# Kernel optimization log

Measured on AMD Instinct MI355X. Metric: run time of the kernel, lower is better.

Reference implementation:

```python
import jax, jax.numpy as jnp
import numpy as np

BLOCK = 128
QMAX = 127.0


def act_quant(x2d):
    # Per (row, 128-wide block) symmetric int8 quantization.
    # x2d: [M, K] -> q int8-valued [M, K], scales [M, K//BLOCK]
    M, K = x2d.shape
    xb = x2d.reshape(M, K // BLOCK, BLOCK)
    s = jnp.max(jnp.abs(xb), axis=-1) / QMAX            # [M, K//BLOCK]
    s = jnp.maximum(s, 1e-12)
    q = jnp.clip(jnp.round(xb / s[..., None]), -128.0, 127.0)
    return q, s  # q kept in fp32 (exact small ints)


def weight_quant(w):
    # w: [N, K] -> q [N, K], scales [N//BLOCK, K//BLOCK]
    N, K = w.shape
    wb = w.reshape(N // BLOCK, BLOCK, K // BLOCK, BLOCK)
    s = jnp.max(jnp.abs(wb), axis=(1, 3)) / QMAX        # [N//BLOCK, K//BLOCK]
    s = jnp.maximum(s, 1e-12)
    q = jnp.clip(jnp.round(wb / s[:, None, :, None]), -128.0, 127.0)
    return q.reshape(N, K), s


def setup_inputs() -> dict:
    key = jax.random.key(0)
    k1, k2, k3 = jax.random.split(key, 3)
    x = jax.random.normal(k1, (4, 2048, 4096), dtype=jnp.float32)
    weight = jax.random.normal(k2, (4096, 4096), dtype=jnp.float32) * 0.02
    bias = jax.random.normal(k3, (4096,), dtype=jnp.float32) * 0.02
    return {"x": x, "weight": weight, "bias": bias}


def reference(x, weight, bias):
    # Int8Linear.forward: block-quantize activation, int8 GEMM with
    # grouped dequant scales (equivalent to dequantize-then-matmul), add bias.
    orig_shape = x.shape
    K = weight.shape[1]
    N = weight.shape[0]
    x2d = x.reshape(-1, K)                              # [M, K]
    M = x2d.shape[0]

    xq, xs = act_quant(x2d)                             # [M,Kb,128], [M,Kb]
    wq, ws = weight_quant(weight)                       # [N,K],     [Nb,Kb]

    # Dequantize (exact factorization of the scaled int8 GEMM):
    # out[m,n] = sum_kb xs[m,kb]*ws[nb,kb] * sum_c xq[m,kb,c]*wq[n,kb,c]
    x_dq = (xq * xs[..., None]).reshape(M, K)
    wqb = wq.reshape(N // BLOCK, BLOCK, K // BLOCK, BLOCK)
    w_dq = (wqb * ws[:, None, :, None]).reshape(N, K)

    out = x_dq @ w_dq.T + bias                          # [M, N]
    return out.reshape(orig_shape[:-1] + (N,))
```

## Files before the change

kernel.cpp:

```cpp
#include <hip/hip_runtime.h>
#include <stdint.h>

#define K_DIM 4096
#define N_DIM 4096
#define KB    32
#define QMAXF 127.0f

typedef int v4i __attribute__((ext_vector_type(4)));

__device__ __forceinline__ void async_copy16(void* lds, const void* gptr) {
    __builtin_amdgcn_global_load_lds(
        (__attribute__((address_space(1))) void*)gptr,
        (__attribute__((address_space(3))) void*)lds, 16, 0, 0);
}

__global__ __launch_bounds__(256) void act_quant_kernel(
    const float* __restrict__ x, int8_t* __restrict__ xq,
    float* __restrict__ xs_t, int M)
{
    const int m = blockIdx.x;
    const int t = threadIdx.x;
    const float* xrow = x + (size_t)m * K_DIM;
    int8_t* qrow = xq + (size_t)m * K_DIM;

#pragma unroll
    for (int p = 0; p < 4; ++p) {
        const int base = p * 1024 + t * 4;
        float4 v = *(const float4*)(xrow + base);
        float a = fmaxf(fmaxf(fabsf(v.x), fabsf(v.y)), fmaxf(fabsf(v.z), fabsf(v.w)));
#pragma unroll
        for (int off = 1; off < 32; off <<= 1)
            a = fmaxf(a, __shfl_xor(a, off, 64));
        const float s = fmaxf(a / QMAXF, 1e-12f);
        const float inv = 1.0f / s;
        float q0 = fminf(fmaxf(rintf(v.x * inv), -128.f), 127.f);
        float q1 = fminf(fmaxf(rintf(v.y * inv), -128.f), 127.f);
        float q2 = fminf(fmaxf(rintf(v.z * inv), -128.f), 127.f);
        float q3 = fminf(fmaxf(rintf(v.w * inv), -128.f), 127.f);
        char4 pk;
        pk.x = (char)(int)q0; pk.y = (char)(int)q1;
        pk.z = (char)(int)q2; pk.w = (char)(int)q3;
        *(char4*)(qrow + base) = pk;
        if ((t & 31) == 0) {
            const int g = base >> 7;
            xs_t[(size_t)g * M + m] = s;
        }
    }
}

__global__ __launch_bounds__(256) void weight_quant_kernel(
    const float* __restrict__ w, int8_t* __restrict__ wq, float* __restrict__ ws)
{
    const int nb = blockIdx.x >> 5;
    const int kb = blockIdx.x & 31;
    const int t  = threadIdx.x;
    const int n0 = nb * 128, k0 = kb * 128;

    float4 vals[16];
    float a = 0.f;
#pragma unroll
    for (int ii = 0; ii < 16; ++ii) {
        const int e = ii * 1024 + t * 4;
        const int row = e >> 7, col = e & 127;
        float4 v = *(const float4*)(w + (size_t)(n0 + row) * K_DIM + k0 + col);
        vals[ii] = v;
        a = fmaxf(a, fmaxf(fmaxf(fabsf(v.x), fabsf(v.y)), fmaxf(fabsf(v.z), fabsf(v.w))));
    }
#pragma unroll
    for (int off = 1; off < 64; off <<= 1)
        a = fmaxf(a, __shfl_xor(a, off, 64));
    __shared__ float wred[4];
    if ((t & 63) == 0) wred[t >> 6] = a;
    __syncthreads();
    a = fmaxf(fmaxf(wred[0], wred[1]), fmaxf(wred[2], wred[3]));
    const float s = fmaxf(a / QMAXF, 1e-12f);
    const float inv = 1.0f / s;
    if (t == 0) ws[nb * KB + kb] = s;

#pragma unroll
    for (int ii = 0; ii < 16; ++ii) {
        const int e = ii * 1024 + t * 4;
        const int row = e >> 7, col = e & 127;
        float4 v = vals[ii];
        char4 pk;
        pk.x = (char)(int)fminf(fmaxf(rintf(v.x * inv), -128.f), 127.f);
        pk.y = (char)(int)fminf(fmaxf(rintf(v.y * inv), -128.f), 127.f);
        pk.z = (char)(int)fminf(fmaxf(rintf(v.z * inv), -128.f), 127.f);
        pk.w = (char)(int)fminf(fmaxf(rintf(v.w * inv), -128.f), 127.f);
        *(char4*)(wq + (size_t)(n0 + row) * K_DIM + k0 + col) = pk;
    }
}

__global__ __launch_bounds__(256, 3) void gemm_kernel(
    const int8_t* __restrict__ xq, const int8_t* __restrict__ wq,
    const float* __restrict__ xs_t, const float* __restrict__ ws,
    const float* __restrict__ bias, float* __restrict__ out, int M)
{
    __shared__ __align__(16) int8_t As[128 * 128];
    __shared__ __align__(16) int8_t Bs[128 * 128];
    __shared__ __align__(16) float  xs_s[KB * 128];
    __shared__ float ws_s[KB];

    const int t    = threadIdx.x;
    const int lane = t & 63;
    const int wave = t >> 6;
    const int nb   = blockIdx.x;
    const int n0   = nb * 128;
    const int m0   = blockIdx.y * 128;

#pragma unroll
    for (int i = 0; i < 4; ++i) {
        const int idx = t * 4 + i * 1024;
        const int kbi = idx >> 7, r = idx & 127;
        *(float4*)&xs_s[idx] = *(const float4*)&xs_t[(size_t)kbi * M + m0 + r];
    }
    if (t < KB) ws_s[t] = ws[nb * KB + t];

    const int wm    = (wave >> 1) * 64;
    const int wn    = (wave & 1) * 64;
    const int frow  = lane & 15;
    const int q     = lane >> 4;
    const int quad4 = q * 4;
    const int sw0   = ((q ^ (frow & 7)) * 16);

    float4 facc[4][4] = {};

    float bj[4];
#pragma unroll
    for (int j = 0; j < 4; ++j) bj[j] = bias[n0 + wn + j * 16 + frow];

    for (int kb = 0; kb < KB; ++kb) {
        __syncthreads();
        const int8_t* Ag = xq + (size_t)m0 * K_DIM + kb * 128;
        const int8_t* Bg = wq + (size_t)n0 * K_DIM + kb * 128;
#pragma unroll
        for (int it = 0; it < 4; ++it) {
            const int ci  = it * 256 + t;
            const int row = ci >> 3;
            const int c   = (ci & 7) ^ (row & 7);
            void* la = (void*)&As[(it * 256 + wave * 64) * 16];
            void* lb = (void*)&Bs[(it * 256 + wave * 64) * 16];
            async_copy16(la, Ag + (size_t)row * K_DIM + c * 16);
            async_copy16(lb, Bg + (size_t)row * K_DIM + c * 16);
        }
        __syncthreads();

        v4i a0[4], a1[4], b0[4], b1[4];
#pragma unroll
        for (int i = 0; i < 4; ++i) {
            a0[i] = *(const v4i*)&As[(wm + i * 16 + frow) * 128 + sw0];
            a1[i] = *(const v4i*)&As[(wm + i * 16 + frow) * 128 + (sw0 ^ 64)];
            b0[i] = *(const v4i*)&Bs[(wn + i * 16 + frow) * 128 + sw0];
            b1[i] = *(const v4i*)&Bs[(wn + i * 16 + frow) * 128 + (sw0 ^ 64)];
        }
        const float wskb = ws_s[kb];
#pragma unroll
        for (int i = 0; i < 4; ++i) {
            float4 xs4 = *(const float4*)&xs_s[kb * 128 + wm + i * 16 + quad4];
            const float s0 = xs4.x * wskb, s1 = xs4.y * wskb;
            const float s2 = xs4.z * wskb, s3 = xs4.w * wskb;
#pragma unroll
            for (int j = 0; j < 4; ++j) {
                v4i d = __builtin_amdgcn_mfma_i32_16x16x64_i8(a0[i], b0[j], (v4i){0, 0, 0, 0}, 0, 0, 0);
                d = __builtin_amdgcn_mfma_i32_16x16x64_i8(a1[i], b1[j], d, 0, 0, 0);
                facc[i][j].x += (float)d[0] * s0;
                facc[i][j].y += (float)d[1] * s1;
                facc[i][j].z += (float)d[2] * s2;
                facc[i][j].w += (float)d[3] * s3;
            }
        }
    }

#pragma unroll
    for (int i = 0; i < 4; ++i) {
#pragma unroll
        for (int r = 0; r < 4; ++r) {
            const int row = m0 + wm + i * 16 + quad4 + r;
            float* orow = out + (size_t)row * N_DIM + n0 + wn + frow;
#pragma unroll
            for (int j = 0; j < 4; ++j)
                orow[j * 16] = ((const float*)&facc[i][j])[r] + bj[j];
        }
    }
}

extern "C" void kernel_launch(void* const* d_in, const int* in_sizes, int n_in,
                              void* d_out, int out_size, void* d_ws, size_t ws_size,
                              hipStream_t stream)
{
    const float* x    = (const float*)d_in[0];
    const float* w    = (const float*)d_in[1];
    const float* bias = (const float*)d_in[2];
    float* out = (float*)d_out;
    const int M = in_sizes[0] / K_DIM;

    int8_t* xq  = (int8_t*)d_ws;
    int8_t* wqp = xq + (size_t)M * K_DIM;
    float*  xst = (float*)(wqp + (size_t)N_DIM * K_DIM);
    float*  wsp = xst + (size_t)KB * M;

    act_quant_kernel<<<M, 256, 0, stream>>>(x, xq, xst, M);
    weight_quant_kernel<<<(N_DIM / 128) * KB, 256, 0, stream>>>(w, wqp, wsp);
    gemm_kernel<<<dim3(N_DIM / 128, M / 128), 256, 0, stream>>>(
        xq, wqp, xst, wsp, bias, out, M);
}
```

Baseline: 446.1 us.

## Enlarge GEMM tile to 256x128 and batch activation-quant loads

The GEMM block tile grows from 128x128 to 256x128 rows. Each wave now computes 128x64 with 8x4 accumulators, so each loaded B tile is reused across twice as many rows and per-FLOP global/LDS traffic drops. Bias is folded into the accumulator init, and the scale accumulation uses explicit FMA. The activation quant kernel processes two rows per block and issues all eight loads before reducing, to raise memory-level parallelism. The cost is more registers and LDS per block, lowering occupancy (launch bounds go from 3 to 2) and leaving half as many GEMM blocks in the grid.

Measured after the change: 549.2 us. 1.23x slower.

```diff
diff --git a/kernel.cpp b/kernel.cpp
--- a/kernel.cpp
+++ b/kernel.cpp
@@ -18,31 +18,35 @@
     const float* __restrict__ x, int8_t* __restrict__ xq,
     float* __restrict__ xs_t, int M)
 {
-    const int m = blockIdx.x;
-    const int t = threadIdx.x;
+    const int t   = threadIdx.x;
+    const int r   = t >> 7;
+    const int tid = t & 127;
+    const int m   = blockIdx.x * 2 + r;
     const float* xrow = x + (size_t)m * K_DIM;
     int8_t* qrow = xq + (size_t)m * K_DIM;
 
-#pragma unroll
-    for (int p = 0; p < 4; ++p) {
-        const int base = p * 1024 + t * 4;
-        float4 v = *(const float4*)(xrow + base);
-        float a = fmaxf(fmaxf(fabsf(v.x), fabsf(v.y)), fmaxf(fabsf(v.z), fabsf(v.w)));
+    float4 v[8];
+#pragma unroll
+    for (int p = 0; p < 8; ++p)
+        v[p] = *(const float4*)(xrow + p * 512 + tid * 4);
+
+#pragma unroll
+    for (int p = 0; p < 8; ++p) {
+        float a = fmaxf(fmaxf(fabsf(v[p].x), fabsf(v[p].y)),
+                        fmaxf(fabsf(v[p].z), fabsf(v[p].w)));
 #pragma unroll
         for (int off = 1; off < 32; off <<= 1)
             a = fmaxf(a, __shfl_xor(a, off, 64));
         const float s = fmaxf(a / QMAXF, 1e-12f);
         const float inv = 1.0f / s;
-        float q0 = fminf(fmaxf(rintf(v.x * inv), -128.f), 127.f);
-        float q1 = fminf(fmaxf(rintf(v.y * inv), -128.f), 127.f);
-        float q2 = fminf(fmaxf(rintf(v.z * inv), -128.f), 127.f);
-        float q3 = fminf(fmaxf(rintf(v.w * inv), -128.f), 127.f);
         char4 pk;
-        pk.x = (char)(int)q0; pk.y = (char)(int)q1;
-        pk.z = (char)(int)q2; pk.w = (char)(int)q3;
-        *(char4*)(qrow + base) = pk;
-        if ((t & 31) == 0) {
-            const int g = base >> 7;
+        pk.x = (char)(int)fminf(fmaxf(rintf(v[p].x * inv), -128.f), 127.f);
+        pk.y = (char)(int)fminf(fmaxf(rintf(v[p].y * inv), -128.f), 127.f);
+        pk.z = (char)(int)fminf(fmaxf(rintf(v[p].z * inv), -128.f), 127.f);
+        pk.w = (char)(int)fminf(fmaxf(rintf(v[p].w * inv), -128.f), 127.f);
+        *(char4*)(qrow + p * 512 + tid * 4) = pk;
+        if ((tid & 31) == 0) {
+            const int g = p * 4 + (tid >> 5);
             xs_t[(size_t)g * M + m] = s;
         }
     }
@@ -91,14 +95,14 @@
     }
 }
 
-__global__ __launch_bounds__(256, 3) void gemm_kernel(
+__global__ __launch_bounds__(256, 2) void gemm_kernel(
     const int8_t* __restrict__ xq, const int8_t* __restrict__ wq,
     const float* __restrict__ xs_t, const float* __restrict__ ws,
     const float* __restrict__ bias, float* __restrict__ out, int M)
 {
-    __shared__ __align__(16) int8_t As[128 * 128];
+    __shared__ __align__(16) int8_t As[256 * 128];
     __shared__ __align__(16) int8_t Bs[128 * 128];
-    __shared__ __align__(16) float  xs_s[KB * 128];
+    __shared__ __align__(16) float  xs_s[KB * 256];
     __shared__ float ws_s[KB];
 
     const int t    = threadIdx.x;
@@ -106,80 +110,89 @@
     const int wave = t >> 6;
     const int nb   = blockIdx.x;
     const int n0   = nb * 128;
-    const int m0   = blockIdx.y * 128;
-
-#pragma unroll
-    for (int i = 0; i < 4; ++i) {
+    const int m0   = blockIdx.y * 256;
+
+#pragma unroll
+    for (int i = 0; i < 8; ++i) {
         const int idx = t * 4 + i * 1024;
-        const int kbi = idx >> 7, r = idx & 127;
+        const int kbi = idx >> 8, r = idx & 255;
         *(float4*)&xs_s[idx] = *(const float4*)&xs_t[(size_t)kbi * M + m0 + r];
     }
     if (t < KB) ws_s[t] = ws[nb * KB + t];
 
-    const int wm    = (wave >> 1) * 64;
+    const int wm    = (wave >> 1) * 128;
     const int wn    = (wave & 1) * 64;
     const int frow  = lane & 15;
     const int q     = lane >> 4;
     const int quad4 = q * 4;
-    const int sw0   = ((q ^ (frow & 7)) * 16);
-
-    float4 facc[4][4] = {};
-
-    float bj[4];
-#pragma unroll
-    for (int j = 0; j < 4; ++j) bj[j] = bias[n0 + wn + j * 16 + frow];
+    const int sw0   = (q ^ (frow & 7)) * 16;
+
+    float4 facc[8][4];
+#pragma unroll
+    for (int j = 0; j < 4; ++j) {
+        const float b = bias[n0 + wn + j * 16 + frow];
+#pragma unroll
+        for (int i = 0; i < 8; ++i)
+            facc[i][j] = (float4){b, b, b, b};
+    }
 
     for (int kb = 0; kb < KB; ++kb) {
         __syncthreads();
         const int8_t* Ag = xq + (size_t)m0 * K_DIM + kb * 128;
         const int8_t* Bg = wq + (size_t)n0 * K_DIM + kb * 128;
 #pragma unroll
+        for (int it = 0; it < 8; ++it) {
+            const int ci  = it * 256 + t;
+            const int row = ci >> 3;
+            const int c   = (ci & 7) ^ (row & 7);
+            async_copy16((void*)&As[(it * 256 + wave * 64) * 16],
+                         Ag + (size_t)row * K_DIM + c * 16);
+        }
+#pragma unroll
         for (int it = 0; it < 4; ++it) {
             const int ci  = it * 256 + t;
             const int row = ci >> 3;
             const int c   = (ci & 7) ^ (row & 7);
-            void* la = (void*)&As[(it * 256 + wave * 64) * 16];
-            void* lb = (void*)&Bs[(it * 256 + wave * 64) * 16];
-            async_copy16(la, Ag + (size_t)row * K_DIM + c * 16);
-            async_copy16(lb, Bg + (size_t)row * K_DIM + c * 16);
+            async_copy16((void*)&Bs[(it * 256 + wave * 64) * 16],
+                         Bg + (size_t)row * K_DIM + c * 16);
         }
         __syncthreads();
 
-        v4i a0[4], a1[4], b0[4], b1[4];
-#pragma unroll
-        for (int i = 0; i < 4; ++i) {
-            a0[i] = *(const v4i*)&As[(wm + i * 16 + frow) * 128 + sw0];
-            a1[i] = *(const v4i*)&As[(wm + i * 16 + frow) * 128 + (sw0 ^ 64)];
-            b0[i] = *(const v4i*)&Bs[(wn + i * 16 + frow) * 128 + sw0];
-            b1[i] = *(const v4i*)&Bs[(wn + i * 16 + frow) * 128 + (sw0 ^ 64)];
+        v4i b0[4], b1[4];
+#pragma unroll
+        for (int j = 0; j < 4; ++j) {
+            b0[j] = *(const v4i*)&Bs[(wn + j * 16 + frow) * 128 + sw0];
+            b1[j] = *(const v4i*)&Bs[(wn + j * 16 + frow) * 128 + (sw0 ^ 64)];
         }
         const float wskb = ws_s[kb];
 #pragma unroll
-        for (int i = 0; i < 4; ++i) {
-            float4 xs4 = *(const float4*)&xs_s[kb * 128 + wm + i * 16 + quad4];
+        for (int i = 0; i < 8; ++i) {
+            const v4i a0 = *(const v4i*)&As[(wm + i * 16 + frow) * 128 + sw0];
+            const v4i a1 = *(const v4i*)&As[(wm + i * 16 + frow) * 128 + (sw0 ^ 64)];
+            float4 xs4 = *(const float4*)&xs_s[kb * 256 + wm + i * 16 + quad4];
             const float s0 = xs4.x * wskb, s1 = xs4.y * wskb;
             const float s2 = xs4.z * wskb, s3 = xs4.w * wskb;
 #pragma unroll
             for (int j = 0; j < 4; ++j) {
-                v4i d = __builtin_amdgcn_mfma_i32_16x16x64_i8(a0[i], b0[j], (v4i){0, 0, 0, 0}, 0, 0, 0);
-                d = __builtin_amdgcn_mfma_i32_16x16x64_i8(a1[i], b1[j], d, 0, 0, 0);
-                facc[i][j].x += (float)d[0] * s0;
-                facc[i][j].y += (float)d[1] * s1;
-                facc[i][j].z += (float)d[2] * s2;
-                facc[i][j].w += (float)d[3] * s3;
+                v4i d = __builtin_amdgcn_mfma_i32_16x16x64_i8(a0, b0[j], (v4i){0, 0, 0, 0}, 0, 0, 0);
+                d = __builtin_amdgcn_mfma_i32_16x16x64_i8(a1, b1[j], d, 0, 0, 0);
+                facc[i][j].x = __builtin_fmaf((float)d[0], s0, facc[i][j].x);
+                facc[i][j].y = __builtin_fmaf((float)d[1], s1, facc[i][j].y);
+                facc[i][j].z = __builtin_fmaf((float)d[2], s2, facc[i][j].z);
+                facc[i][j].w = __builtin_fmaf((float)d[3], s3, facc[i][j].w);
             }
         }
     }
 
 #pragma unroll
-    for (int i = 0; i < 4; ++i) {
+    for (int i = 0; i < 8; ++i) {
 #pragma unroll
         for (int r = 0; r < 4; ++r) {
             const int row = m0 + wm + i * 16 + quad4 + r;
             float* orow = out + (size_t)row * N_DIM + n0 + wn + frow;
 #pragma unroll
             for (int j = 0; j < 4; ++j)
-                orow[j * 16] = ((const float*)&facc[i][j])[r] + bj[j];
+                orow[j * 16] = ((const float*)&facc[i][j])[r];
         }
     }
 }
@@ -199,8 +212,8 @@
     float*  xst = (float*)(wqp + (size_t)N_DIM * K_DIM);
     float*  wsp = xst + (size_t)KB * M;
 
-    act_quant_kernel<<<M, 256, 0, stream>>>(x, xq, xst, M);
+    act_quant_kernel<<<M / 2, 256, 0, stream>>>(x, xq, xst, M);
     weight_quant_kernel<<<(N_DIM / 128) * KB, 256, 0, stream>>>(w, wqp, wsp);
-    gemm_kernel<<<dim3(N_DIM / 128, M / 128), 256, 0, stream>>>(
+    gemm_kernel<<<dim3(N_DIM / 128, M / 256), 256, 0, stream>>>(
         xq, wqp, xst, wsp, bias, out, M);
 }
```
